# Kernel tuning notes

Hardware: AMD Instinct MI355X
Metric: run time of the kernel (lower is better)

The kernel has to match this reference:

```python
import jax, jax.numpy as jnp
import numpy as np

D_MODEL = 512
NUM_EXPERTS = 8
TOP_K = 2
FFN = 2048
H = 2 * D_MODEL            # GRU hidden per direction
GRU_OUT = 4 * D_MODEL      # bidirectional concat
B, T = 8, 1024
BAL_W, Z_W = 0.01, 0.001


def setup_inputs() -> dict:
    key = jax.random.key(0)
    ks = jax.random.split(key, 12)
    s = 1.0 / np.sqrt(H)  # torch GRU uniform init scale
    u = lambda k, shape: jax.random.uniform(k, shape, jnp.float32, -s, s)
    tn = lambda k, shape: jax.random.normal(k, shape, jnp.float32) * 0.02
    return {
        "x": jax.random.normal(ks[0], (B, T, D_MODEL), jnp.float32),
        # GRU params, stacked [2 directions, ...]; gate order (r, z, n) as in torch
        "gru_Wih": u(ks[1], (2, 3 * H, D_MODEL)),
        "gru_Whh": u(ks[2], (2, 3 * H, H)),
        "gru_bih": u(ks[3], (2, 3 * H)),
        "gru_bhh": u(ks[4], (2, 3 * H)),
        "gate_W": tn(ks[5], (NUM_EXPERTS, GRU_OUT)),
        "gate_b": jnp.zeros((NUM_EXPERTS,), jnp.float32),
        "W1": tn(ks[6], (NUM_EXPERTS, GRU_OUT, FFN)),
        "b1": jnp.zeros((NUM_EXPERTS, FFN), jnp.float32),
        "W2": tn(ks[7], (NUM_EXPERTS, FFN, D_MODEL)),
        "b2": jnp.zeros((NUM_EXPERTS, D_MODEL), jnp.float32),
    }


def _gru_bidir(x, Wih, Whh, bih, bhh):
    # x: [B,T,D]; returns [B,T,2H]
    Bn = x.shape[0]

    def run(d, reverse):
        # precompute input projections: [T,B,3H]
        xg = jnp.swapaxes(jnp.einsum('btd,gd->btg', x, Wih[d]) + bih[d], 0, 1)
        Whh_d, bhh_d = Whh[d], bhh[d]

        def step(h, xt):
            hg = h @ Whh_d.T + bhh_d
            xr, xz, xn = jnp.split(xt, 3, axis=-1)
            hr, hz, hn = jnp.split(hg, 3, axis=-1)
            r = jax.nn.sigmoid(xr + hr)
            z = jax.nn.sigmoid(xz + hz)
            n = jnp.tanh(xn + r * hn)
            h_new = (1.0 - z) * n + z * h
            return h_new, h_new

        h0 = jnp.zeros((Bn, H), x.dtype)
        _, ys = jax.lax.scan(step, h0, xg, reverse=reverse)  # ys[t] aligned with time t
        return jnp.swapaxes(ys, 0, 1)

    return jnp.concatenate([run(0, False), run(1, True)], axis=-1)


def reference(x, gru_Wih, gru_Whh, gru_bih, gru_bhh, gate_W, gate_b, W1, b1, W2, b2):
    Bn, Tn, _ = x.shape
    n = Bn * Tn
    E = NUM_EXPERTS

    gru_out = _gru_bidir(x, gru_Wih, gru_Whh, gru_bih, gru_bhh)
    gru_out = jax.nn.leaky_relu(gru_out, 0.01)          # dropout=0.0 -> identity
    flat = gru_out.reshape(n, GRU_OUT)

    # gating (expert_bias buffer is zeros at init)
    logits = flat @ gate_W.T + gate_b                    # [n,E]
    z_loss = Z_W * jnp.mean(jnp.square(jax.nn.logsumexp(logits, axis=-1)))
    scores = jax.nn.softmax(logits, axis=-1)
    top_scores, top_idx = jax.lax.top_k(scores, TOP_K)   # [n,K]
    weights = top_scores / jnp.sum(top_scores, axis=-1, keepdims=True)

    expert_mask = jnp.sum(jax.nn.one_hot(top_idx, E, dtype=jnp.float32), axis=1)  # [n,E]
    f = jax.lax.stop_gradient(jnp.mean(expert_mask, axis=0))
    P = jnp.mean(scores, axis=0)
    balance_loss = BAL_W * E * jnp.sum(f * P)
    aux_loss = balance_loss + z_loss

    # masked-dense expert combine (math identical to gather/scatter loop)
    output = jnp.zeros((n, D_MODEL), jnp.float32)
    for e in range(E):
        h = jax.nn.gelu(flat @ W1[e] + b1[e], approximate=False)  # [n,FFN]
        out_e = h @ W2[e] + b2[e]                                 # [n,D]
        w_e = jnp.sum(weights * (top_idx == e), axis=-1)          # [n]
        output = output + w_e[:, None] * out_e

    return output.reshape(Bn, Tn, D_MODEL).astype(x.dtype), aux_loss
```

## Files before the change

kernel.cpp:

```cpp
#include <hip/hip_runtime.h>
#include <math.h>

#define NTOK 8192
#define DM   512
#define HID  1024
#define G3H  3072
#define GOUT 2048
#define FFND 2048
#define NEXP 8

#define XG_OFF    0ULL
#define HG_OFF    0ULL
#define OG_OFF    134217728ULL
#define FLAT_OFF  201326592ULL
#define HBUF_OFF  268435456ULL
#define FLAGS_OFF 268566528ULL
#define IMETA_OFF 268567552ULL
#define FMETA_OFF 268571648ULL
#define TKIDX_OFF 268575744ULL
#define TKW_OFF   268641280ULL
#define PAIRT_OFF 268706816ULL
#define PAIRW_OFF 268772352ULL
#define SLOT_OFF  268837888ULL

__global__ void k0_init(float* p) {
    int i = blockIdx.x * 256 + threadIdx.x;
    if (i < 35072) p[i] = 0.f;
}

__global__ __launch_bounds__(256, 2) void k1_sgemm_bt(
    const float* __restrict__ A, const float* __restrict__ B,
    const float* __restrict__ bias, float* __restrict__ C) {
    __shared__ float As[16 * 132];
    __shared__ float Bs[16 * 132];
    const int tid = threadIdx.x;
    const int m0 = blockIdx.y * 128;
    const int n0 = blockIdx.x * 128;
    const int tx = tid & 15, ty = tid >> 4;
    const int arow = tid >> 2, ac4 = (tid & 3) * 4;
    float acc[8][8];
#pragma unroll
    for (int i = 0; i < 8; ++i)
#pragma unroll
        for (int j = 0; j < 8; ++j) acc[i][j] = 0.f;

    for (int k0 = 0; k0 < 512; k0 += 16) {
        __syncthreads();
#pragma unroll
        for (int r = 0; r < 2; ++r) {
            int row = r * 64 + arow;
            float4 va = *(const float4*)(A + (size_t)(m0 + row) * 512 + k0 + ac4);
            As[(ac4 + 0) * 132 + row] = va.x;
            As[(ac4 + 1) * 132 + row] = va.y;
            As[(ac4 + 2) * 132 + row] = va.z;
            As[(ac4 + 3) * 132 + row] = va.w;
            float4 vb = *(const float4*)(B + (size_t)(n0 + row) * 512 + k0 + ac4);
            Bs[(ac4 + 0) * 132 + row] = vb.x;
            Bs[(ac4 + 1) * 132 + row] = vb.y;
            Bs[(ac4 + 2) * 132 + row] = vb.z;
            Bs[(ac4 + 3) * 132 + row] = vb.w;
        }
        __syncthreads();
#pragma unroll
        for (int k = 0; k < 16; ++k) {
            float4 a0 = *(const float4*)&As[k * 132 + ty * 8];
            float4 a1 = *(const float4*)&As[k * 132 + ty * 8 + 4];
            float4 b0 = *(const float4*)&Bs[k * 132 + tx * 8];
            float4 b1 = *(const float4*)&Bs[k * 132 + tx * 8 + 4];
            float av[8] = {a0.x, a0.y, a0.z, a0.w, a1.x, a1.y, a1.z, a1.w};
            float bv[8] = {b0.x, b0.y, b0.z, b0.w, b1.x, b1.y, b1.z, b1.w};
#pragma unroll
            for (int i = 0; i < 8; ++i)
#pragma unroll
                for (int j = 0; j < 8; ++j) acc[i][j] = fmaf(av[i], bv[j], acc[i][j]);
        }
    }
    float4 c0 = *(const float4*)(bias + n0 + tx * 8);
    float4 c1 = *(const float4*)(bias + n0 + tx * 8 + 4);
    float bb[8] = {c0.x, c0.y, c0.z, c0.w, c1.x, c1.y, c1.z, c1.w};
#pragma unroll
    for (int i = 0; i < 8; ++i) {
        float* op = C + (size_t)(m0 + ty * 8 + i) * 6144 + n0 + tx * 8;
        float4 o0 = make_float4(acc[i][0] + bb[0], acc[i][1] + bb[1],
                                acc[i][2] + bb[2], acc[i][3] + bb[3]);
        float4 o1 = make_float4(acc[i][4] + bb[4], acc[i][5] + bb[5],
                                acc[i][6] + bb[6], acc[i][7] + bb[7]);
        *(float4*)op = o0;
        *(float4*)(op + 4) = o1;
    }
}

__global__ __launch_bounds__(256) void k2_gru(
    const float* __restrict__ Whh, const float* __restrict__ bhh,
    const float* __restrict__ xg, float* __restrict__ flat,
    float* __restrict__ hbuf, int* __restrict__ flags) {
    __shared__ float Wl[1024 * 24];
    __shared__ float red[32 * 200];
    __shared__ float s2[192];
    const int tid = threadIdx.x;
    const int dir = blockIdx.x >> 7;
    const int wg = blockIdx.x & 127;
    const int j0 = wg * 8;
    const float* W0 = Whh + (size_t)dir * G3H * HID;
    for (int idx = tid; idx < 24 * 1024; idx += 256) {
        int r = idx >> 10, k = idx & 1023;
        int g = r >> 3, u = r & 7;
        Wl[k * 24 + r] = W0[(size_t)(g * 1024 + j0 + u) * 1024 + k];
    }
    const int lane = tid & 63;
    const int b = tid & 7;
    const int kc = tid >> 3;
    const int kb = kc * 32;
    float* hb = hbuf + dir * 16384;
    int* fl = flags + dir * 128;
    float bhh_r = 0.f;
    if (tid < 192) {
        int r = tid >> 3;
        int g = r >> 3, u = r & 7;
        bhh_r = bhh[dir * G3H + g * 1024 + j0 + u];
    }
    const float4* wbase[6];
    int qrow[6];
#pragma unroll
    for (int m = 0; m < 6; ++m) {
        int q = (m + kc) % 6;
        qrow[m] = q * 4;
        wbase[m] = (const float4*)&Wl[kb * 24 + q * 4];
    }
    __syncthreads();

    for (int s = 1; s <= 1024; ++s) {
        const int te = dir ? (1024 - s) : (s - 1);
        float xr = 0.f, xz = 0.f, xn = 0.f;
        if (tid < 64) {
            int u = tid >> 3, bb2 = tid & 7;
            const float* xp = xg + (size_t)(bb2 * 1024 + te) * 6144 + dir * G3H + j0 + u;
            xr = xp[0];
            xz = xp[1024];
            xn = xp[2048];
        }
        if (s > 1) {
            const int c0 = s - 1;
            int it = 0;
            for (;;) {
                int f0 = __hip_atomic_load(fl + lane, __ATOMIC_RELAXED, __HIP_MEMORY_SCOPE_AGENT);
                int f1 = __hip_atomic_load(fl + 64 + lane, __ATOMIC_RELAXED, __HIP_MEMORY_SCOPE_AGENT);
                if (__all((f0 >= c0) && (f1 >= c0))) break;
                if (++it > (1 << 22)) break;
                __builtin_amdgcn_s_sleep(1);
            }
        }
        const float* hp = hb + ((s - 1) & 1) * 8192;
        float hreg[32];
#pragma unroll
        for (int i = 0; i < 32; ++i)
            hreg[i] = __hip_atomic_load(hp + (kb + i) * 8 + b,
                                        __ATOMIC_RELAXED, __HIP_MEMORY_SCOPE_AGENT);
        float hpg = 0.f;
        if (tid < 64)
            hpg = __hip_atomic_load(hp + (j0 + (tid >> 3)) * 8 + (tid & 7),
                                    __ATOMIC_RELAXED, __HIP_MEMORY_SCOPE_AGENT);

        float4 acc[6];
#pragma unroll
        for (int m = 0; m < 6; ++m) acc[m] = make_float4(0.f, 0.f, 0.f, 0.f);
#pragma unroll
        for (int i = 0; i < 32; ++i) {
            float hv = hreg[i];
#pragma unroll
            for (int m = 0; m < 6; ++m) {
                float4 wv = wbase[m][i * 6];
                acc[m].x = fmaf(wv.x, hv, acc[m].x);
                acc[m].y = fmaf(wv.y, hv, acc[m].y);
                acc[m].z = fmaf(wv.z, hv, acc[m].z);
                acc[m].w = fmaf(wv.w, hv, acc[m].w);
            }
        }
#pragma unroll
        for (int m = 0; m < 6; ++m) {
            float* rp = &red[kc * 200 + qrow[m] * 8 + b];
            rp[0] = acc[m].x;
            rp[8] = acc[m].y;
            rp[16] = acc[m].z;
            rp[24] = acc[m].w;
        }
        __syncthreads();
        if (tid < 192) {
            float sum = 0.f;
#pragma unroll
            for (int kk = 0; kk < 32; ++kk) sum += red[kk * 200 + tid];
            s2[tid] = sum + bhh_r;
        }
        __syncthreads();
        float hnew = 0.f;
        int u = tid >> 3, bb2 = tid & 7;
        if (tid < 64) {
            float hr = s2[u * 8 + bb2];
            float hz = s2[(8 + u) * 8 + bb2];
            float hn = s2[(16 + u) * 8 + bb2];
            float rg = 1.f / (1.f + expf(-(xr + hr)));
            float zg = 1.f / (1.f + expf(-(xz + hz)));
            float ng = tanhf(xn + rg * hn);
            hnew = (1.f - zg) * ng + zg * hpg;
            __hip_atomic_store(hb + (s & 1) * 8192 + (j0 + u) * 8 + bb2, hnew,
                               __ATOMIC_RELAXED, __HIP_MEMORY_SCOPE_AGENT);
        }
        if (tid < 64) {
            __builtin_amdgcn_s_waitcnt(0);
            if (tid == 0)
                __hip_atomic_store(fl + wg, s, __ATOMIC_RELAXED, __HIP_MEMORY_SCOPE_AGENT);
            float lr = hnew > 0.f ? hnew : 0.01f * hnew;
            flat[(size_t)(bb2 * 1024 + te) * 2048 + dir * 1024 + j0 + u] = lr;
        }
    }
}

__global__ __launch_bounds__(256) void k3_gate(
    const float* __restrict__ flat, const float* __restrict__ gate_W,
    const float* __restrict__ gate_b,
    int* __restrict__ tk_idx, float* __restrict__ tk_w,
    int* __restrict__ counts, float* __restrict__ fmeta) {
    __shared__ float gw[8 * 2048];
    __shared__ float bP[9];
    __shared__ int bC[8];
    const int tid = threadIdx.x;
    for (int i = tid; i < 8 * 2048; i += 256) gw[i] = gate_W[i];
    if (tid < 9) bP[tid] = 0.f;
    if (tid < 8) bC[tid] = 0;
    __syncthreads();
    const int lane = tid & 63, w = tid >> 6;
    const int tbase = blockIdx.x * 16 + w * 4;
    for (int j = 0; j < 4; ++j) {
        int t = tbase + j;
        const float* fr = flat + (size_t)t * 2048;
        float a[8];
#pragma unroll
        for (int e = 0; e < 8; ++e) a[e] = 0.f;
        for (int i = 0; i < 32; ++i) {
            float v = fr[i * 64 + lane];
#pragma unroll
            for (int e = 0; e < 8; ++e) a[e] = fmaf(v, gw[e * 2048 + i * 64 + lane], a[e]);
        }
#pragma unroll
        for (int e = 0; e < 8; ++e) {
#pragma unroll
            for (int off = 32; off > 0; off >>= 1) a[e] += __shfl_down(a[e], off);
        }
        if (lane == 0) {
            float lg[8];
#pragma unroll
            for (int e = 0; e < 8; ++e) lg[e] = a[e] + gate_b[e];
            float m = lg[0];
#pragma unroll
            for (int e = 1; e < 8; ++e) m = fmaxf(m, lg[e]);
            float sc[8], ssum = 0.f;
#pragma unroll
            for (int e = 0; e < 8; ++e) { sc[e] = expf(lg[e] - m); ssum += sc[e]; }
            float inv = 1.f / ssum;
#pragma unroll
            for (int e = 0; e < 8; ++e) sc[e] *= inv;
            float lse = m + logf(ssum);
            int i1 = 0; float s1 = sc[0];
#pragma unroll
            for (int e = 1; e < 8; ++e) if (sc[e] > s1) { s1 = sc[e]; i1 = e; }
            int i2 = (i1 == 0) ? 1 : 0; float s2v = sc[i2];
#pragma unroll
            for (int e = 0; e < 8; ++e) if (e != i1 && sc[e] > s2v) { s2v = sc[e]; i2 = e; }
            float wsum = s1 + s2v;
            tk_idx[2 * t] = i1; tk_idx[2 * t + 1] = i2;
            tk_w[2 * t] = s1 / wsum; tk_w[2 * t + 1] = s2v / wsum;
            atomicAdd(&bC[i1], 1);
            atomicAdd(&bC[i2], 1);
#pragma unroll
            for (int e = 0; e < 8; ++e) atomicAdd(&bP[e], sc[e]);
            atomicAdd(&bP[8], lse * lse);
        }
    }
    __syncthreads();
    if (tid < 8) {
        atomicAdd(&counts[tid], bC[tid]);
        atomicAdd(&fmeta[tid], bP[tid]);
    }
    if (tid == 8) atomicAdd(&fmeta[8], bP[8]);
}

__global__ void k4_sched(int* im, float* fm, float* aux_out) {
    int tid = threadIdx.x;
    if (tid < 136) { im[32 + tid] = -1; im[168 + tid] = 0; }
    __syncthreads();
    if (tid == 0) {
        int off = 0;
        for (int e = 0; e < 8; ++e) { im[16 + e] = off; im[8 + e] = off; off += im[e]; }
        im[24] = off;
        int T = 0;
        for (int e = 0; e < 8; ++e) {
            int c = im[e], o = im[16 + e];
            for (int i = 0; i < c; i += 128) { im[32 + T] = e; im[168 + T] = o + i; ++T; }
        }
        im[25] = T;
        float fP = 0.f;
        for (int e = 0; e < 8; ++e) fP += ((float)im[e] / 8192.f) * (fm[e] / 8192.f);
        *aux_out = 0.01f * 8.f * fP + 0.001f * (fm[8] / 8192.f);
    }
}

__global__ __launch_bounds__(256) void k5_scatter(
    const int* __restrict__ tk_idx, const float* __restrict__ tk_w,
    int* __restrict__ im, int* __restrict__ pair_t,
    float* __restrict__ pair_w, int* __restrict__ slot) {
    __shared__ int cnt[8], base[8];
    const int tid = threadIdx.x;
    if (tid < 8) cnt[tid] = 0;
    __syncthreads();
    const int t = blockIdx.x * 256 + tid;
    const int e0 = tk_idx[2 * t], e1 = tk_idx[2 * t + 1];
    const int p0 = atomicAdd(&cnt[e0], 1);
    const int p1 = atomicAdd(&cnt[e1], 1);
    __syncthreads();
    if (tid < 8) base[tid] = atomicAdd(&im[8 + tid], cnt[tid]);
    __syncthreads();
    const int q0 = base[e0] + p0, q1 = base[e1] + p1;
    pair_t[q0] = t; pair_w[q0] = tk_w[2 * t];     slot[2 * t] = q0;
    pair_t[q1] = t; pair_w[q1] = tk_w[2 * t + 1]; slot[2 * t + 1] = q1;
}

__global__ __launch_bounds__(256, 2) void k6_ffn1(
    const float* __restrict__ flat, const float* __restrict__ W1,
    const float* __restrict__ b1, const int* __restrict__ im,
    const int* __restrict__ pair_t, float* __restrict__ Hg) {
    const int rt = blockIdx.x % 136;
    const int nt = blockIdx.x / 136;
    const int e = im[32 + rt];
    if (e < 0) return;
    const int pStart = im[168 + rt];
    const int pEnd = im[16 + e + 1];
    __shared__ float As[16 * 132];
    __shared__ float Bs[16 * 132];
    const int tid = threadIdx.x;
    const int tx = tid & 15, ty = tid >> 4;
    const int n0 = nt * 128;
    const float* Bb = W1 + (size_t)e * 2048 * 2048;
    const int arow = tid >> 2, ac4 = (tid & 3) * 4;
    const int bk = tid >> 4, bn = (tid & 15) * 8;
    int r0 = pStart + arow;       if (r0 > pEnd - 1) r0 = pEnd - 1;
    int r1 = pStart + 64 + arow;  if (r1 > pEnd - 1) r1 = pEnd - 1;
    const float* arp0 = flat + (size_t)pair_t[r0] * 2048;
    const float* arp1 = flat + (size_t)pair_t[r1] * 2048;
    float acc[8][8];
#pragma unroll
    for (int i = 0; i < 8; ++i)
#pragma unroll
        for (int j = 0; j < 8; ++j) acc[i][j] = 0.f;

    for (int k0 = 0; k0 < 2048; k0 += 16) {
        __syncthreads();
        {
            float4 va = *(const float4*)(arp0 + k0 + ac4);
            As[(ac4 + 0) * 132 + arow] = va.x;
            As[(ac4 + 1) * 132 + arow] = va.y;
            As[(ac4 + 2) * 132 + arow] = va.z;
            As[(ac4 + 3) * 132 + arow] = va.w;
            float4 vb = *(const float4*)(arp1 + k0 + ac4);
            As[(ac4 + 0) * 132 + 64 + arow] = vb.x;
            As[(ac4 + 1) * 132 + 64 + arow] = vb.y;
            As[(ac4 + 2) * 132 + 64 + arow] = vb.z;
            As[(ac4 + 3) * 132 + 64 + arow] = vb.w;
            float4 w0 = *(const float4*)(Bb + (size_t)(k0 + bk) * 2048 + n0 + bn);
            float4 w1 = *(const float4*)(Bb + (size_t)(k0 + bk) * 2048 + n0 + bn + 4);
            *(float4*)&Bs[bk * 132 + bn] = w0;
            *(float4*)&Bs[bk * 132 + bn + 4] = w1;
        }
        __syncthreads();
#pragma unroll
        for (int k = 0; k < 16; ++k) {
            float4 a0 = *(const float4*)&As[k * 132 + ty * 8];
            float4 a1 = *(const float4*)&As[k * 132 + ty * 8 + 4];
            float4 b0 = *(const float4*)&Bs[k * 132 + tx * 8];
            float4 b1v = *(const float4*)&Bs[k * 132 + tx * 8 + 4];
            float av[8] = {a0.x, a0.y, a0.z, a0.w, a1.x, a1.y, a1.z, a1.w};
            float bv[8] = {b0.x, b0.y, b0.z, b0.w, b1v.x, b1v.y, b1v.z, b1v.w};
#pragma unroll
            for (int i = 0; i < 8; ++i)
#pragma unroll
                for (int j = 0; j < 8; ++j) acc[i][j] = fmaf(av[i], bv[j], acc[i][j]);
        }
    }
    float4 c0 = *(const float4*)(b1 + (size_t)e * 2048 + n0 + tx * 8);
    float4 c1 = *(const float4*)(b1 + (size_t)e * 2048 + n0 + tx * 8 + 4);
    float bb[8] = {c0.x, c0.y, c0.z, c0.w, c1.x, c1.y, c1.z, c1.w};
#pragma unroll
    for (int i = 0; i < 8; ++i) {
        int p = pStart + ty * 8 + i;
        if (p < pEnd) {
            float* op = Hg + (size_t)p * 2048 + n0 + tx * 8;
            float o[8];
#pragma unroll
            for (int j = 0; j < 8; ++j) {
                float xv = acc[i][j] + bb[j];
                o[j] = 0.5f * xv * (1.f + erff(xv * 0.70710678118654752f));
            }
            *(float4*)op = make_float4(o[0], o[1], o[2], o[3]);
            *(float4*)(op + 4) = make_float4(o[4], o[5], o[6], o[7]);
        }
    }
}

__global__ __launch_bounds__(256, 2) void k7_ffn2(
    const float* __restrict__ Hg, const float* __restrict__ W2,
    const float* __restrict__ b2, const int* __restrict__ im,
    float* __restrict__ Og) {
    const int rt = blockIdx.x % 136;
    const int nt = blockIdx.x / 136;
    const int e = im[32 + rt];
    if (e < 0) return;
    const int pStart = im[168 + rt];
    const int pEnd = im[16 + e + 1];
    __shared__ float As[16 * 132];
    __shared__ float Bs[16 * 132];
    const int tid = threadIdx.x;
    const int tx = tid & 15, ty = tid >> 4;
    const int n0 = nt * 128;
    const float* Bb = W2 + (size_t)e * 2048 * 512;
    const int arow = tid >> 2, ac4 = (tid & 3) * 4;
    const int bk = tid >> 4, bn = (tid & 15) * 8;
    int r0 = pStart + arow;       if (r0 > pEnd - 1) r0 = pEnd - 1;
    int r1 = pStart + 64 + arow;  if (r1 > pEnd - 1) r1 = pEnd - 1;
    const float* arp0 = Hg + (size_t)r0 * 2048;
    const float* arp1 = Hg + (size_t)r1 * 2048;
    float acc[8][8];
#pragma unroll
    for (int i = 0; i < 8; ++i)
#pragma unroll
        for (int j = 0; j < 8; ++j) acc[i][j] = 0.f;

    for (int k0 = 0; k0 < 2048; k0 += 16) {
        __syncthreads();
        {
            float4 va = *(const float4*)(arp0 + k0 + ac4);
            As[(ac4 + 0) * 132 + arow] = va.x;
            As[(ac4 + 1) * 132 + arow] = va.y;
            As[(ac4 + 2) * 132 + arow] = va.z;
            As[(ac4 + 3) * 132 + arow] = va.w;
            float4 vb = *(const float4*)(arp1 + k0 + ac4);
            As[(ac4 + 0) * 132 + 64 + arow] = vb.x;
            As[(ac4 + 1) * 132 + 64 + arow] = vb.y;
            As[(ac4 + 2) * 132 + 64 + arow] = vb.z;
            As[(ac4 + 3) * 132 + 64 + arow] = vb.w;
            float4 w0 = *(const float4*)(Bb + (size_t)(k0 + bk) * 512 + n0 + bn);
            float4 w1 = *(const float4*)(Bb + (size_t)(k0 + bk) * 512 + n0 + bn + 4);
            *(float4*)&Bs[bk * 132 + bn] = w0;
            *(float4*)&Bs[bk * 132 + bn + 4] = w1;
        }
        __syncthreads();
#pragma unroll
        for (int k = 0; k < 16; ++k) {
            float4 a0 = *(const float4*)&As[k * 132 + ty * 8];
            float4 a1 = *(const float4*)&As[k * 132 + ty * 8 + 4];
            float4 b0 = *(const float4*)&Bs[k * 132 + tx * 8];
            float4 b1v = *(const float4*)&Bs[k * 132 + tx * 8 + 4];
            float av[8] = {a0.x, a0.y, a0.z, a0.w, a1.x, a1.y, a1.z, a1.w};
            float bv[8] = {b0.x, b0.y, b0.z, b0.w, b1v.x, b1v.y, b1v.z, b1v.w};
#pragma unroll
            for (int i = 0; i < 8; ++i)
#pragma unroll
                for (int j = 0; j < 8; ++j) acc[i][j] = fmaf(av[i], bv[j], acc[i][j]);
        }
    }
    float4 c0 = *(const float4*)(b2 + (size_t)e * 512 + n0 + tx * 8);
    float4 c1 = *(const float4*)(b2 + (size_t)e * 512 + n0 + tx * 8 + 4);
    float bb[8] = {c0.x, c0.y, c0.z, c0.w, c1.x, c1.y, c1.z, c1.w};
#pragma unroll
    for (int i = 0; i < 8; ++i) {
        int p = pStart + ty * 8 + i;
        if (p < pEnd) {
            float* op = Og + (size_t)p * 512 + n0 + tx * 8;
            *(float4*)op = make_float4(acc[i][0] + bb[0], acc[i][1] + bb[1],
                                       acc[i][2] + bb[2], acc[i][3] + bb[3]);
            *(float4*)(op + 4) = make_float4(acc[i][4] + bb[4], acc[i][5] + bb[5],
                                             acc[i][6] + bb[6], acc[i][7] + bb[7]);
        }
    }
}

__global__ __launch_bounds__(256) void k8_comb(
    const float* __restrict__ Og, const int* __restrict__ slot,
    const float* __restrict__ pw, float* __restrict__ out) {
    const int i4 = blockIdx.x * 256 + threadIdx.x;
    const int t = i4 >> 7;
    const int d = (i4 & 127) << 2;
    const int s0 = slot[2 * t], s1 = slot[2 * t + 1];
    const float w0 = pw[s0], w1 = pw[s1];
    float4 a = *(const float4*)(Og + (size_t)s0 * 512 + d);
    float4 b = *(const float4*)(Og + (size_t)s1 * 512 + d);
    float4 o = make_float4(w0 * a.x + w1 * b.x, w0 * a.y + w1 * b.y,
                           w0 * a.z + w1 * b.z, w0 * a.w + w1 * b.w);
    *(float4*)(out + (size_t)t * 512 + d) = o;
}

extern "C" void kernel_launch(void* const* d_in, const int* in_sizes, int n_in,
                              void* d_out, int out_size, void* d_ws, size_t ws_size,
                              hipStream_t stream) {
    (void)in_sizes; (void)n_in; (void)out_size; (void)ws_size;
    const float* x   = (const float*)d_in[0];
    const float* Wih = (const float*)d_in[1];
    const float* Whh = (const float*)d_in[2];
    const float* bih = (const float*)d_in[3];
    const float* bhh = (const float*)d_in[4];
    const float* gW  = (const float*)d_in[5];
    const float* gb  = (const float*)d_in[6];
    const float* W1  = (const float*)d_in[7];
    const float* b1  = (const float*)d_in[8];
    const float* W2  = (const float*)d_in[9];
    const float* b2  = (const float*)d_in[10];
    float* out = (float*)d_out;
    char* ws = (char*)d_ws;
    float* xg    = (float*)(ws + XG_OFF);
    float* Hg    = (float*)(ws + HG_OFF);
    float* Og    = (float*)(ws + OG_OFF);
    float* flat  = (float*)(ws + FLAT_OFF);
    float* hbuf  = (float*)(ws + HBUF_OFF);
    int*   flags = (int*)(ws + FLAGS_OFF);
    int*   im    = (int*)(ws + IMETA_OFF);
    float* fm    = (float*)(ws + FMETA_OFF);
    int*   tki   = (int*)(ws + TKIDX_OFF);
    float* tkw   = (float*)(ws + TKW_OFF);
    int*   prt   = (int*)(ws + PAIRT_OFF);
    float* prw   = (float*)(ws + PAIRW_OFF);
    int*   slt   = (int*)(ws + SLOT_OFF);

    hipLaunchKernelGGL(k0_init, dim3(138), dim3(256), 0, stream, (float*)(ws + HBUF_OFF));
    hipLaunchKernelGGL(k1_sgemm_bt, dim3(48, 64), dim3(256), 0, stream, x, Wih, bih, xg);
    hipLaunchKernelGGL(k2_gru, dim3(256), dim3(256), 0, stream, Whh, bhh, xg, flat, hbuf, flags);
    hipLaunchKernelGGL(k3_gate, dim3(512), dim3(256), 0, stream, flat, gW, gb, tki, tkw, im, fm);
    hipLaunchKernelGGL(k4_sched, dim3(1), dim3(256), 0, stream, im, fm, out + 4194304);
    hipLaunchKernelGGL(k5_scatter, dim3(32), dim3(256), 0, stream, tki, tkw, im, prt, prw, slt);
    hipLaunchKernelGGL(k6_ffn1, dim3(136 * 16), dim3(256), 0, stream, flat, W1, b1, im, prt, Hg);
    hipLaunchKernelGGL(k7_ffn2, dim3(136 * 4), dim3(256), 0, stream, Hg, W2, b2, im, Og);
    hipLaunchKernelGGL(k8_comb, dim3(4096), dim3(256), 0, stream, Og, slt, prw, out);
}
```

Measured before the change: 11.59 ms.

## Replace GRU flag barrier with parity-bit tagged hidden state and register-resident weights

The persistent GRU kernel no longer polls a per-workgroup flag array before each step. It tags the low mantissa bit of each stored hidden value with step parity, and readers spin per element until the expected parity appears, so data and readiness travel together. Recurrent weights now live in registers instead of LDS, the hidden vector is staged into swizzled LDS, and the k-reduction is split over 64 chunks. The trade-offs are a one-bit precision loss in the hidden state, higher register pressure, and reuse of the top-k index buffer as the second direction's hidden buffer.

```diff
diff --git a/kernel.cpp b/kernel.cpp
--- a/kernel.cpp
+++ b/kernel.cpp
@@ -23,9 +23,16 @@
 #define PAIRW_OFF 268772352ULL
 #define SLOT_OFF  268837888ULL
 
-__global__ void k0_init(float* p) {
+__global__ void k0_init(char* ws) {
     int i = blockIdx.x * 256 + threadIdx.x;
-    if (i < 35072) p[i] = 0.f;
+    if (i < 16384) {
+        ((unsigned*)(ws + HBUF_OFF))[i] = (i < 8192) ? 0u : 1u;
+    } else if (i < 32768) {
+        int j = i - 16384;
+        ((unsigned*)(ws + TKIDX_OFF))[j] = (j < 8192) ? 0u : 1u;
+    } else {
+        ((float*)(ws + IMETA_OFF))[i - 32768] = 0.f;
+    }
 }
 
 __global__ __launch_bounds__(256, 2) void k1_sgemm_bt(
@@ -93,124 +100,137 @@
 __global__ __launch_bounds__(256) void k2_gru(
     const float* __restrict__ Whh, const float* __restrict__ bhh,
     const float* __restrict__ xg, float* __restrict__ flat,
-    float* __restrict__ hbuf, int* __restrict__ flags) {
-    __shared__ float Wl[1024 * 24];
-    __shared__ float red[32 * 200];
-    __shared__ float s2[192];
+    float* hb0, float* hb1) {
+    __shared__ float hlsf[8192];
+    __shared__ float red[64 * 196];
+    __shared__ float s2b[192];
+    char* hls = (char*)hlsf;
     const int tid = threadIdx.x;
     const int dir = blockIdx.x >> 7;
     const int wg = blockIdx.x & 127;
-    const int j0 = wg * 8;
+    const int j0 = wg << 3;
+    float* hbd = dir ? hb1 : hb0;
+    const int rg = tid >> 6;
+    const int kc = tid & 63;
+    const int swz = (kc & 7) << 4;
+
     const float* W0 = Whh + (size_t)dir * G3H * HID;
-    for (int idx = tid; idx < 24 * 1024; idx += 256) {
-        int r = idx >> 10, k = idx & 1023;
-        int g = r >> 3, u = r & 7;
-        Wl[k * 24 + r] = W0[(size_t)(g * 1024 + j0 + u) * 1024 + k];
-    }
-    const int lane = tid & 63;
-    const int b = tid & 7;
-    const int kc = tid >> 3;
-    const int kb = kc * 32;
-    float* hb = hbuf + dir * 16384;
-    int* fl = flags + dir * 128;
+    float wreg[6][16];
+#pragma unroll
+    for (int rr = 0; rr < 6; ++rr) {
+        const int r = rg * 6 + rr;
+        const float* wp = W0 + (size_t)(((r >> 3) << 10) + j0 + (r & 7)) * 1024 + (kc << 4);
+        const float4 w0 = ((const float4*)wp)[0];
+        const float4 w1 = ((const float4*)wp)[1];
+        const float4 w2 = ((const float4*)wp)[2];
+        const float4 w3 = ((const float4*)wp)[3];
+        wreg[rr][0] = w0.x;  wreg[rr][1] = w0.y;  wreg[rr][2] = w0.z;  wreg[rr][3] = w0.w;
+        wreg[rr][4] = w1.x;  wreg[rr][5] = w1.y;  wreg[rr][6] = w1.z;  wreg[rr][7] = w1.w;
+        wreg[rr][8] = w2.x;  wreg[rr][9] = w2.y;  wreg[rr][10] = w2.z; wreg[rr][11] = w2.w;
+        wreg[rr][12] = w3.x; wreg[rr][13] = w3.y; wreg[rr][14] = w3.z; wreg[rr][15] = w3.w;
+    }
     float bhh_r = 0.f;
     if (tid < 192) {
-        int r = tid >> 3;
-        int g = r >> 3, u = r & 7;
-        bhh_r = bhh[dir * G3H + g * 1024 + j0 + u];
-    }
-    const float4* wbase[6];
-    int qrow[6];
-#pragma unroll
-    for (int m = 0; m < 6; ++m) {
-        int q = (m + kc) % 6;
-        qrow[m] = q * 4;
-        wbase[m] = (const float4*)&Wl[kb * 24 + q * 4];
-    }
-    __syncthreads();
+        const int r = tid >> 3;
+        bhh_r = bhh[dir * G3H + ((r >> 3) << 10) + j0 + (r & 7)];
+    }
+    const int u = tid >> 3, bb = tid & 7;
+    float hprev = 0.f;
 
     for (int s = 1; s <= 1024; ++s) {
         const int te = dir ? (1024 - s) : (s - 1);
         float xr = 0.f, xz = 0.f, xn = 0.f;
         if (tid < 64) {
-            int u = tid >> 3, bb2 = tid & 7;
-            const float* xp = xg + (size_t)(bb2 * 1024 + te) * 6144 + dir * G3H + j0 + u;
+            const float* xp = xg + (size_t)((bb << 10) + te) * 6144 + dir * G3H + j0 + u;
             xr = xp[0];
             xz = xp[1024];
             xn = xp[2048];
         }
-        if (s > 1) {
-            const int c0 = s - 1;
-            int it = 0;
-            for (;;) {
-                int f0 = __hip_atomic_load(fl + lane, __ATOMIC_RELAXED, __HIP_MEMORY_SCOPE_AGENT);
-                int f1 = __hip_atomic_load(fl + 64 + lane, __ATOMIC_RELAXED, __HIP_MEMORY_SCOPE_AGENT);
-                if (__all((f0 >= c0) && (f1 >= c0))) break;
-                if (++it > (1 << 22)) break;
-                __builtin_amdgcn_s_sleep(1);
+        float* src = hbd + (((s - 1) & 1) << 13);
+        float hv[32];
+#pragma unroll
+        for (int i = 0; i < 32; ++i)
+            hv[i] = __hip_atomic_load(src + (i << 8) + tid,
+                                      __ATOMIC_RELAXED, __HIP_MEMORY_SCOPE_AGENT);
+        const unsigned exbit = (((unsigned)(s - 1)) >> 1) & 1u;
+#pragma unroll
+        for (int i = 0; i < 32; ++i) {
+            if ((__float_as_uint(hv[i]) & 1u) != exbit) {
+                int gx = 0;
+                do {
+                    __builtin_amdgcn_s_sleep(2);
+                    hv[i] = __hip_atomic_load(src + (i << 8) + tid,
+                                              __ATOMIC_RELAXED, __HIP_MEMORY_SCOPE_AGENT);
+                } while (((__float_as_uint(hv[i]) & 1u) != exbit) && (++gx < (1 << 20)));
             }
         }
-        const float* hp = hb + ((s - 1) & 1) * 8192;
-        float hreg[32];
-#pragma unroll
-        for (int i = 0; i < 32; ++i)
-            hreg[i] = __hip_atomic_load(hp + (kb + i) * 8 + b,
-                                        __ATOMIC_RELAXED, __HIP_MEMORY_SCOPE_AGENT);
-        float hpg = 0.f;
-        if (tid < 64)
-            hpg = __hip_atomic_load(hp + (j0 + (tid >> 3)) * 8 + (tid & 7),
-                                    __ATOMIC_RELAXED, __HIP_MEMORY_SCOPE_AGENT);
-
-        float4 acc[6];
-#pragma unroll
-        for (int m = 0; m < 6; ++m) acc[m] = make_float4(0.f, 0.f, 0.f, 0.f);
 #pragma unroll
         for (int i = 0; i < 32; ++i) {
-            float hv = hreg[i];
-#pragma unroll
-            for (int m = 0; m < 6; ++m) {
-                float4 wv = wbase[m][i * 6];
-                acc[m].x = fmaf(wv.x, hv, acc[m].x);
-                acc[m].y = fmaf(wv.y, hv, acc[m].y);
-                acc[m].z = fmaf(wv.z, hv, acc[m].z);
-                acc[m].w = fmaf(wv.w, hv, acc[m].w);
+            const int p = (i << 8) + tid;
+            const int k = p >> 3;
+            const int off = (((k << 5) + ((p & 7) << 2))) ^ (((k >> 4) & 7) << 4);
+            *(float*)(hls + off) = hv[i];
+        }
+        __syncthreads();
+        float acc[6][8];
+#pragma unroll
+        for (int rr = 0; rr < 6; ++rr)
+#pragma unroll
+            for (int q = 0; q < 8; ++q) acc[rr][q] = 0.f;
+#pragma unroll
+        for (int i = 0; i < 16; ++i) {
+            const int kbase = ((kc << 4) + i) << 5;
+            const float4 hA = *(const float4*)(hls + (kbase ^ swz));
+            const float4 hB = *(const float4*)(hls + ((kbase + 16) ^ swz));
+#pragma unroll
+            for (int rr = 0; rr < 6; ++rr) {
+                const float w = wreg[rr][i];
+                acc[rr][0] = fmaf(w, hA.x, acc[rr][0]);
+                acc[rr][1] = fmaf(w, hA.y, acc[rr][1]);
+                acc[rr][2] = fmaf(w, hA.z, acc[rr][2]);
+                acc[rr][3] = fmaf(w, hA.w, acc[rr][3]);
+                acc[rr][4] = fmaf(w, hB.x, acc[rr][4]);
+                acc[rr][5] = fmaf(w, hB.y, acc[rr][5]);
+                acc[rr][6] = fmaf(w, hB.z, acc[rr][6]);
+                acc[rr][7] = fmaf(w, hB.w, acc[rr][7]);
             }
         }
-#pragma unroll
-        for (int m = 0; m < 6; ++m) {
-            float* rp = &red[kc * 200 + qrow[m] * 8 + b];
-            rp[0] = acc[m].x;
-            rp[8] = acc[m].y;
-            rp[16] = acc[m].z;
-            rp[24] = acc[m].w;
+        float* rp = red + kc * 196 + rg * 48;
+#pragma unroll
+        for (int rr = 0; rr < 6; ++rr) {
+            *(float4*)(rp + (rr << 3)) =
+                make_float4(acc[rr][0], acc[rr][1], acc[rr][2], acc[rr][3]);
+            *(float4*)(rp + (rr << 3) + 4) =
+                make_float4(acc[rr][4], acc[rr][5], acc[rr][6], acc[rr][7]);
         }
         __syncthreads();
         if (tid < 192) {
-            float sum = 0.f;
-#pragma unroll
-            for (int kk = 0; kk < 32; ++kk) sum += red[kk * 200 + tid];
-            s2[tid] = sum + bhh_r;
-        }
-        __syncthreads();
-        float hnew = 0.f;
-        int u = tid >> 3, bb2 = tid & 7;
+            float a0 = 0.f, a1 = 0.f, a2 = 0.f, a3 = 0.f;
+#pragma unroll
+            for (int q = 0; q < 64; q += 4) {
+                a0 += red[(q + 0) * 196 + tid];
+                a1 += red[(q + 1) * 196 + tid];
+                a2 += red[(q + 2) * 196 + tid];
+                a3 += red[(q + 3) * 196 + tid];
+            }
+            s2b[tid] = (a0 + a1) + (a2 + a3) + bhh_r;
+        }
+        __syncthreads();
         if (tid < 64) {
-            float hr = s2[u * 8 + bb2];
-            float hz = s2[(8 + u) * 8 + bb2];
-            float hn = s2[(16 + u) * 8 + bb2];
-            float rg = 1.f / (1.f + expf(-(xr + hr)));
-            float zg = 1.f / (1.f + expf(-(xz + hz)));
-            float ng = tanhf(xn + rg * hn);
-            hnew = (1.f - zg) * ng + zg * hpg;
-            __hip_atomic_store(hb + (s & 1) * 8192 + (j0 + u) * 8 + bb2, hnew,
+            const float hr = s2b[tid];
+            const float hz = s2b[64 + tid];
+            const float hn = s2b[128 + tid];
+            const float rg_ = 1.f / (1.f + expf(-(xr + hr)));
+            const float zg_ = 1.f / (1.f + expf(-(xz + hz)));
+            const float ng_ = tanhf(xn + rg_ * hn);
+            const float hnew = (1.f - zg_) * ng_ + zg_ * hprev;
+            hprev = hnew;
+            const unsigned hu = (__float_as_uint(hnew) & ~1u) | (((unsigned)s >> 1) & 1u);
+            __hip_atomic_store(hbd + ((s & 1) << 13) + ((j0 + u) << 3) + bb,
+                               __uint_as_float(hu),
                                __ATOMIC_RELAXED, __HIP_MEMORY_SCOPE_AGENT);
-        }
-        if (tid < 64) {
-            __builtin_amdgcn_s_waitcnt(0);
-            if (tid == 0)
-                __hip_atomic_store(fl + wg, s, __ATOMIC_RELAXED, __HIP_MEMORY_SCOPE_AGENT);
-            float lr = hnew > 0.f ? hnew : 0.01f * hnew;
-            flat[(size_t)(bb2 * 1024 + te) * 2048 + dir * 1024 + j0 + u] = lr;
+            const float lr = hnew > 0.f ? hnew : 0.01f * hnew;
+            flat[(size_t)((bb << 10) + te) * 2048 + dir * 1024 + j0 + u] = lr;
         }
     }
 }
@@ -518,8 +538,8 @@
     float* Hg    = (float*)(ws + HG_OFF);
     float* Og    = (float*)(ws + OG_OFF);
     float* flat  = (float*)(ws + FLAT_OFF);
-    float* hbuf  = (float*)(ws + HBUF_OFF);
-    int*   flags = (int*)(ws + FLAGS_OFF);
+    float* hb0   = (float*)(ws + HBUF_OFF);
+    float* hb1   = (float*)(ws + TKIDX_OFF);
     int*   im    = (int*)(ws + IMETA_OFF);
     float* fm    = (float*)(ws + FMETA_OFF);
     int*   tki   = (int*)(ws + TKIDX_OFF);
@@ -528,9 +548,9 @@
     float* prw   = (float*)(ws + PAIRW_OFF);
     int*   slt   = (int*)(ws + SLOT_OFF);
 
-    hipLaunchKernelGGL(k0_init, dim3(138), dim3(256), 0, stream, (float*)(ws + HBUF_OFF));
+    hipLaunchKernelGGL(k0_init, dim3(136), dim3(256), 0, stream, ws);
     hipLaunchKernelGGL(k1_sgemm_bt, dim3(48, 64), dim3(256), 0, stream, x, Wih, bih, xg);
-    hipLaunchKernelGGL(k2_gru, dim3(256), dim3(256), 0, stream, Whh, bhh, xg, flat, hbuf, flags);
+    hipLaunchKernelGGL(k2_gru, dim3(256), dim3(256), 0, stream, Whh, bhh, xg, flat, hb0, hb1);
     hipLaunchKernelGGL(k3_gate, dim3(512), dim3(256), 0, stream, flat, gW, gb, tki, tkw, im, fm);
     hipLaunchKernelGGL(k4_sched, dim3(1), dim3(256), 0, stream, im, fm, out + 4194304);
     hipLaunchKernelGGL(k5_scatter, dim3(32), dim3(256), 0, stream, tki, tkw, im, prt, prw, slt);
```

After: 16.99 ms. 1.47x slower.
